# Optimization experiments

Hardware: AMD Instinct MI355X
Metric: run time of the kernel (lower is better)

The kernel has to match this reference:

```python
import jax, jax.numpy as jnp
import numpy as np

B, D = 65536, 154

def setup_inputs() -> dict:
    key = jax.random.key(0)
    k1, k2, k3, k4, k5, k6 = jax.random.split(key, 6)
    recon_l = jax.random.normal(k1, (B, D), dtype=jnp.float32)
    recon_r = jax.random.normal(k2, (B, D), dtype=jnp.float32)
    KLD_l = jax.random.normal(k3, (B, D), dtype=jnp.float32)
    KLD_r = jax.random.normal(k4, (B, D), dtype=jnp.float32)
    lr = jax.random.randint(k5, (B,), 0, 3, dtype=jnp.int64)
    # f_pose in {-1, 0}: -1 marks invalid samples
    f_pose = jax.random.randint(k6, (B,), 0, 2, dtype=jnp.int64) - 1
    return {"recon_l": recon_l, "recon_r": recon_r, "KLD_l": KLD_l,
            "KLD_r": KLD_r, "lr": lr, "f_pose": f_pose}

def reference(recon_l, recon_r, KLD_l, KLD_r, lr, f_pose):
    valid = (f_pose != -1)
    use_l = (valid & ((lr == 0) | (lr == 2))).astype(recon_l.dtype)  # [B]
    use_r = (valid & ((lr == 1) | (lr == 2))).astype(recon_r.dtype)  # [B]
    # per-sample sums over 154-dim pose params, then masked batch reduction
    recon_loss_all = jnp.dot(use_l, recon_l.sum(axis=1)) + jnp.dot(use_r, recon_r.sum(axis=1))
    KLD_loss_all = jnp.dot(use_l, KLD_l.sum(axis=1)) + jnp.dot(use_r, KLD_r.sum(axis=1))
    count = (use_l.sum() + use_r.sum()).astype(jnp.int32)
    return (recon_loss_all / 154.0, KLD_loss_all, count)
```

## Files before the change

kernel.cpp:

```cpp
#include <hip/hip_runtime.h>


#define BB 65536
#define DD 154
#define N4 (BB * DD / 4)
#define BLOCKS 9856
#define THREADS 256

__global__ void zero_out_kernel(float* __restrict__ out) {
    if (threadIdx.x < 3) out[threadIdx.x] = 0.0f;
}

__device__ __forceinline__ float2 wpair(int l, int f) {
    const bool valid = (f != -1);
    float2 w;
    w.x = (valid && ((l == 0) || (l == 2))) ? 1.0f : 0.0f;
    w.y = (valid && ((l == 1) || (l == 2))) ? 1.0f : 0.0f;
    return w;
}

__global__ __launch_bounds__(THREADS) void pose_partial_kernel(
    const float* __restrict__ recon_l, const float* __restrict__ recon_r,
    const float* __restrict__ kld_l,   const float* __restrict__ kld_r,
    const int* __restrict__ lr,        const int* __restrict__ fp,
    float* __restrict__ ws,            float* __restrict__ out)
{
    const float4* __restrict__ rl4 = (const float4*)recon_l;
    const float4* __restrict__ rr4 = (const float4*)recon_r;
    const float4* __restrict__ kl4 = (const float4*)kld_l;
    const float4* __restrict__ kr4 = (const float4*)kld_r;

    const int i = blockIdx.x * THREADS + threadIdx.x;
    const int h = 2 * i;
    const int r0 = h / 77;
    const int r1 = (h + 1) / 77;

    const float4 a = rl4[i];
    const float4 b = rr4[i];
    const float4 c = kl4[i];
    const float4 d = kr4[i];

    const float2 w0 = wpair(lr[r0], fp[r0]);
    const float2 w1 = wpair(lr[r1], fp[r1]);

    float acc_recon = w0.x * (a.x + a.y) + w1.x * (a.z + a.w)
                    + w0.y * (b.x + b.y) + w1.y * (b.z + b.w);
    float acc_kld   = w0.x * (c.x + c.y) + w1.x * (c.z + c.w)
                    + w0.y * (d.x + d.y) + w1.y * (d.z + d.w);
    float acc_cnt = 0.0f;
    if (i < BB) {
        const float2 w = wpair(lr[i], fp[i]);
        acc_cnt = w.x + w.y;
    }

#pragma unroll
    for (int off = 32; off > 0; off >>= 1) {
        acc_recon += __shfl_down(acc_recon, off, 64);
        acc_kld   += __shfl_down(acc_kld,   off, 64);
        acc_cnt   += __shfl_down(acc_cnt,   off, 64);
    }

    __shared__ float s_recon[4], s_kld[4], s_cnt[4];
    const int wave = threadIdx.x >> 6;
    const int lane = threadIdx.x & 63;
    if (lane == 0) {
        s_recon[wave] = acc_recon;
        s_kld[wave]   = acc_kld;
        s_cnt[wave]   = acc_cnt;
    }
    __syncthreads();

    if (threadIdx.x == 0) {
        const float r = s_recon[0] + s_recon[1] + s_recon[2] + s_recon[3];
        const float k = s_kld[0]   + s_kld[1]   + s_kld[2]   + s_kld[3];
        const float n = s_cnt[0]   + s_cnt[1]   + s_cnt[2]   + s_cnt[3];
        if (ws != nullptr) {
            ws[blockIdx.x]              = r;
            ws[BLOCKS + blockIdx.x]     = k;
            ws[2 * BLOCKS + blockIdx.x] = n;
        } else {
            atomicAdd(&out[0], r * (1.0f / 154.0f));
            atomicAdd(&out[1], k);
            atomicAdd(&out[2], n);
        }
    }
}

__global__ __launch_bounds__(1024) void final_reduce_kernel(
    const float* __restrict__ ws, float* __restrict__ out)
{
    float r = 0.0f, k = 0.0f, n = 0.0f;
    for (int i = threadIdx.x; i < BLOCKS; i += 1024) {
        r += ws[i];
        k += ws[BLOCKS + i];
        n += ws[2 * BLOCKS + i];
    }
#pragma unroll
    for (int off = 32; off > 0; off >>= 1) {
        r += __shfl_down(r, off, 64);
        k += __shfl_down(k, off, 64);
        n += __shfl_down(n, off, 64);
    }
    __shared__ float s_r[16], s_k[16], s_n[16];
    const int wave = threadIdx.x >> 6;
    const int lane = threadIdx.x & 63;
    if (lane == 0) { s_r[wave] = r; s_k[wave] = k; s_n[wave] = n; }
    __syncthreads();
    if (threadIdx.x == 0) {
        float rr = 0.0f, kk = 0.0f, nn = 0.0f;
#pragma unroll
        for (int w = 0; w < 16; ++w) { rr += s_r[w]; kk += s_k[w]; nn += s_n[w]; }
        out[0] = rr * (1.0f / 154.0f);
        out[1] = kk;
        out[2] = nn;
    }
}

extern "C" void kernel_launch(void* const* d_in, const int* in_sizes, int n_in,
                              void* d_out, int out_size, void* d_ws, size_t ws_size,
                              hipStream_t stream) {
    const float* recon_l = (const float*)d_in[0];
    const float* recon_r = (const float*)d_in[1];
    const float* kld_l   = (const float*)d_in[2];
    const float* kld_r   = (const float*)d_in[3];
    const int*   lr      = (const int*)d_in[4];
    const int*   fp      = (const int*)d_in[5];
    float* out = (float*)d_out;

    const bool use_ws = (d_ws != nullptr) &&
                        (ws_size >= (size_t)(3 * BLOCKS) * sizeof(float));
    float* ws = use_ws ? (float*)d_ws : nullptr;

    if (!use_ws) {
        zero_out_kernel<<<1, 64, 0, stream>>>(out);
    }
    pose_partial_kernel<<<BLOCKS, THREADS, 0, stream>>>(
        recon_l, recon_r, kld_l, kld_r, lr, fp, ws, out);
    if (use_ws) {
        final_reduce_kernel<<<1, 1024, 0, stream>>>(ws, out);
    }
}
```

Before: 178.5 us.

## Process four float4 chunks per thread with double-buffered prefetch loads

```diff
diff --git a/kernel.cpp b/kernel.cpp
--- a/kernel.cpp
+++ b/kernel.cpp
@@ -4,8 +4,10 @@
 #define BB 65536
 #define DD 154
 #define N4 (BB * DD / 4)
-#define BLOCKS 9856
 #define THREADS 256
+#define ITERS 4
+#define BLOCKS (N4 / (THREADS * ITERS))
+#define TSTRIDE (BLOCKS * THREADS)
 
 __global__ void zero_out_kernel(float* __restrict__ out) {
     if (threadIdx.x < 3) out[threadIdx.x] = 0.0f;
@@ -30,26 +32,43 @@
     const float4* __restrict__ kl4 = (const float4*)kld_l;
     const float4* __restrict__ kr4 = (const float4*)kld_r;
 
-    const int i = blockIdx.x * THREADS + threadIdx.x;
-    const int h = 2 * i;
-    const int r0 = h / 77;
-    const int r1 = (h + 1) / 77;
+    const int t = blockIdx.x * THREADS + threadIdx.x;
 
-    const float4 a = rl4[i];
-    const float4 b = rr4[i];
-    const float4 c = kl4[i];
-    const float4 d = kr4[i];
+    float4 A[2], Bv[2], Cv[2], Dv[2];
+    A[0]  = rl4[t];           Bv[0] = rr4[t];
+    Cv[0] = kl4[t];           Dv[0] = kr4[t];
+    A[1]  = rl4[t + TSTRIDE]; Bv[1] = rr4[t + TSTRIDE];
+    Cv[1] = kl4[t + TSTRIDE]; Dv[1] = kr4[t + TSTRIDE];
 
-    const float2 w0 = wpair(lr[r0], fp[r0]);
-    const float2 w1 = wpair(lr[r1], fp[r1]);
+    float acc_recon = 0.0f, acc_kld = 0.0f, acc_cnt = 0.0f;
 
-    float acc_recon = w0.x * (a.x + a.y) + w1.x * (a.z + a.w)
-                    + w0.y * (b.x + b.y) + w1.y * (b.z + b.w);
-    float acc_kld   = w0.x * (c.x + c.y) + w1.x * (c.z + c.w)
-                    + w0.y * (d.x + d.y) + w1.y * (d.z + d.w);
-    float acc_cnt = 0.0f;
-    if (i < BB) {
-        const float2 w = wpair(lr[i], fp[i]);
+#pragma unroll
+    for (int k = 0; k < ITERS; ++k) {
+        const int buf = k & 1;
+        const int idx = t + k * TSTRIDE;
+        const int h   = 2 * idx;
+        const int r0  = h / 77;
+        const int r1  = (h + 1) / 77;
+
+        const float2 w0 = wpair(lr[r0], fp[r0]);
+        const float2 w1 = wpair(lr[r1], fp[r1]);
+
+        const float4 a = A[buf], b = Bv[buf], c = Cv[buf], d = Dv[buf];
+
+        if (k + 2 < ITERS) {
+            const int nidx = t + (k + 2) * TSTRIDE;
+            A[buf]  = rl4[nidx];  Bv[buf] = rr4[nidx];
+            Cv[buf] = kl4[nidx];  Dv[buf] = kr4[nidx];
+        }
+
+        acc_recon += w0.x * (a.x + a.y) + w1.x * (a.z + a.w)
+                   + w0.y * (b.x + b.y) + w1.y * (b.z + b.w);
+        acc_kld   += w0.x * (c.x + c.y) + w1.x * (c.z + c.w)
+                   + w0.y * (d.x + d.y) + w1.y * (d.z + d.w);
+    }
+
+    if (t < BB) {
+        const float2 w = wpair(lr[t], fp[t]);
         acc_cnt = w.x + w.y;
     }
 
```

Result: no change. 177.9 us (-0.4%).
